# Kernel tuning notes

Measured on AMD Instinct MI355X. Metric: run time of the kernel, lower is better.

## Reference

```python
import jax, jax.numpy as jnp
import numpy as np

B, N, L, D, S, NL = 8, 4096, 32, 64, 64, 2  # batch, stocks, lookback, d_in, d_state, n_levels


def setup_inputs() -> dict:
    key = jax.random.key(0)
    ks = jax.random.split(key, 8)
    w = lambda k, shp: jax.random.normal(k, shp, jnp.float32) * 0.05
    return {
        "p_seq": jax.random.normal(ks[0], (B, N, L, D), jnp.float32),
        "lp_W": w(ks[1], (NL, D, D)),      "lp_b": jnp.zeros((NL, D), jnp.float32),
        "pW":   w(ks[2], (NL, D, 3 * S)),  "pb":   jnp.zeros((NL, 3 * S), jnp.float32),
        "oW":   w(ks[3], (NL, S, S)),      "ob":   jnp.zeros((NL, S), jnp.float32),
        "rW":   w(ks[4], (NL, S, S)),      "rb":   jnp.zeros((NL, S), jnp.float32),
        "fW":   w(ks[5], (NL * S, 1)),     "fb":   jnp.zeros((1,), jnp.float32),
    }


def _gelu(x):
    return jax.nn.gelu(x, approximate=False)  # torch nn.GELU default is exact (erf)


def reference(p_seq, lp_W, lp_b, pW, pb, oW, ob, rW, rb, fW, fb):
    n_levels = lp_W.shape[0]
    feats = []
    for i in range(n_levels):  # small fixed loop over structurally distinct levels
        # level projection: [b,n,l,d]
        x = jnp.einsum('bnld,de->bnle', p_seq, lp_W[i]) + lp_b[i]
        # input-dependent SSM params (per-timestep Linear == one batched matmul)
        p = jnp.einsum('bnld,de->bnle', x, pW[i]) + pb[i]
        a, b_, c = jnp.split(p, 3, axis=-1)
        a = jax.nn.sigmoid(a)
        xm = x.mean(-1, keepdims=True)  # [b,n,l,1]

        # selective recurrence h_t = a_t * h_{t-1} + b_t * mean(x_t), scanned over time
        a_t = jnp.moveaxis(a, 2, 0)    # [l,b,n,s]
        b_t = jnp.moveaxis(b_, 2, 0)
        xm_t = jnp.moveaxis(xm, 2, 0)

        def step(h, inp):
            at, bt, xmt = inp
            return at * h + bt * xmt, None

        h0 = jnp.zeros(a_t.shape[1:], x.dtype)  # [b,n,s]
        h_last, _ = jax.lax.scan(step, h0, (a_t, b_t, xm_t))

        # only the last timestep's output feeds the head (matches original)
        o_last = _gelu(c[:, :, -1, :] * h_last) @ oW[i] + ob[i]
        last = o_last + x[:, :, -1, :].mean(-1, keepdims=True)
        feats.append(last @ rW[i] + rb[i])

    h = jnp.concatenate(feats, axis=-1)  # [b,n, n_levels*s]
    y = (h @ fW + fb).squeeze(-1)        # [b,n]
    return y
```

## Files before the change

### kernel.cpp

```cpp
#include <hip/hip_runtime.h>
#include <hip/hip_bf16.h>
#include <math.h>

using s16x8  = __attribute__((ext_vector_type(8)))  short;
using f32x16 = __attribute__((ext_vector_type(16))) float;

#define BB 8
#define NN 4096
#define LL 32
#define DD 64
#define SS 64
#define NLV 2

#define GRID_BLKS 768
#define NGROUPS   4096

#define WEXT_OFF 0
#define BIAS_OFF 28672
#define WVEC_OFF 29120
#define SIG_OFF  29248
#define BETA_OFF 29250
#define C0_OFF   29252
#define FRAG_OFF 29256
#define FRAG_LDS_BYTES 49152
#define XM_BYTE_OFF    49152

__global__ void prep1(const float* __restrict__ lpW, const float* __restrict__ lpb,
                      const float* __restrict__ pW,  const float* __restrict__ pb,
                      const float* __restrict__ oW,  const float* __restrict__ ob,
                      const float* __restrict__ rW,  const float* __restrict__ rb,
                      const float* __restrict__ fW,  float* __restrict__ ws) {
    __shared__ float q[64];
    int blk = blockIdx.x;
    int d = threadIdx.x;
    if (blk < 2 * 224) {
        int l = blk / 224, j = blk % 224;
        const float* lpWl = lpW + l * 64 * 64;
        const float* pWl  = pW  + l * 64 * 192;
        float wv;
        if (j < 128) {
            int col = j;
            float acc = 0.f;
            for (int e = 0; e < 64; ++e) acc = fmaf(lpWl[d * 64 + e], pWl[e * 192 + col], acc);
            wv = acc;
            if (d == 0) {
                float bb = pb[l * 192 + col];
                for (int e = 0; e < 64; ++e) bb = fmaf(lpb[l * 64 + e], pWl[e * 192 + col], bb);
                ws[BIAS_OFF + l * 224 + j] = bb;
            }
        } else if (j < 160) {
            float s = 0.f;
            for (int e = 0; e < 64; ++e) s += lpWl[d * 64 + e];
            wv = s * (1.f / 64.f);
            if (d == 0) {
                float ss = 0.f;
                for (int e = 0; e < 64; ++e) ss += lpb[l * 64 + e];
                ws[BIAS_OFF + l * 224 + j] = ss * (1.f / 64.f);
            }
        } else {
            int col = j - 32;
            float acc = 0.f;
            for (int e = 0; e < 64; ++e) acc = fmaf(lpWl[d * 64 + e], pWl[e * 192 + col], acc);
            wv = acc;
            if (d == 0) {
                float bb = pb[l * 192 + col];
                for (int e = 0; e < 64; ++e) bb = fmaf(lpb[l * 64 + e], pWl[e * 192 + col], bb);
                ws[BIAS_OFF + l * 224 + j] = bb;
            }
        }
        ws[WEXT_OFF + (l * 64 + d) * 224 + j] = wv;
    } else {
        int l = blk - 2 * 224;
        float qv = 0.f;
        for (int j2 = 0; j2 < 64; ++j2) qv = fmaf(rW[l * 4096 + d * 64 + j2], fW[l * 64 + j2], qv);
        q[d] = qv;
        __syncthreads();
        float wv = 0.f;
        for (int s = 0; s < 64; ++s) wv = fmaf(oW[l * 4096 + d * 64 + s], q[s], wv);
        ws[WVEC_OFF + l * 64 + d] = wv;
        if (d == 0) { float s = 0.f; for (int i = 0; i < 64; ++i) s += q[i];               ws[SIG_OFF  + l] = s; }
        if (d == 1) { float s = 0.f; for (int i = 0; i < 64; ++i) s += ob[l*64+i] * q[i];  ws[BETA_OFF + l] = s; }
        if (d == 2) { float s = 0.f; for (int i = 0; i < 64; ++i) s += rb[l*64+i] * fW[l*64+i]; ws[C0_OFF + l] = s; }
    }
}

__global__ void prep2(float* __restrict__ ws) {
    int blk = blockIdx.x;
    int l = blk / 28, r = blk % 28, nt = r / 4, ks = r % 4;
    int lane = threadIdx.x;
    const float* W = ws + WEXT_OFF + l * 64 * 224;
    s16x8 vh;
#pragma unroll
    for (int i = 0; i < 8; ++i) {
        int k   = ks * 16 + ((lane >> 5) << 2) + (i & 3) + ((i >> 2) << 3);
        int col = nt * 32 + (lane & 31);
        unsigned u = __float_as_uint(W[k * 224 + col]);
        unsigned rn = u + 0x7fffu + ((u >> 16) & 1u);
        vh[i] = (short)(rn >> 16);
    }
    size_t dst;
    if (nt == 4) {
        dst = (size_t)XM_BYTE_OFF + ((size_t)l * 4 + ks) * 1024;
    } else {
        int ntp = (nt < 4) ? nt : nt - 1;
        dst = (((size_t)l * 6 + ntp) * 4 + ks) * 1024;
    }
    char* base = reinterpret_cast<char*>(ws) + (size_t)FRAG_OFF * 4 + dst + lane * 16;
    *reinterpret_cast<s16x8*>(base) = vh;
}

#define BFRD(l, ntp, ks) (*reinterpret_cast<const s16x8*>(smem + ((((l)*6+(ntp))*4+(ks)))*1024 + lane16))

#define ACCINIT(acc, bval) do { float _b = (bval); _Pragma("unroll") \
    for (int _r = 0; _r < 16; ++_r) acc[_r] = _b; } while (0)

#define MMP(l, ntA, ntB, accA, accB) do { _Pragma("unroll") \
    for (int ks = 0; ks < 4; ++ks) { \
        s16x8 bA = BFRD(l, ntA, ks), bB = BFRD(l, ntB, ks); \
        accA = __builtin_amdgcn_mfma_f32_32x32x16_bf16(Ah[ks], bA, accA, 0, 0, 0); \
        accB = __builtin_amdgcn_mfma_f32_32x32x16_bf16(Ah[ks], bB, accB, 0, 0, 0); \
    } } while (0)

#define MX1G(l, acc) do { _Pragma("unroll") \
    for (int ks = 0; ks < 4; ++ks) { \
        s16x8 b = FXM[((l)*4+ks)*64 + lane]; \
        acc = __builtin_amdgcn_mfma_f32_32x32x16_bf16(Ah[ks], b, acc, 0, 0, 0); \
    } } while (0)

__global__ __launch_bounds__(512, 4) void mlm_mfma(
    const float* __restrict__ p_seq, const float* __restrict__ fb,
    const float* __restrict__ ws, float* __restrict__ out) {

    __shared__ __align__(16) char smem[FRAG_LDS_BYTES];
    const int tid  = threadIdx.x;
    const int lane = tid & 63;
    const int wv   = tid >> 6;
    const int lane16 = lane * 16;
    const int row  = lane & 31;
    const int kofs = (lane >> 5) * 4;
    const int myhalf = lane >> 5;
    const int col  = lane & 31;

    const s16x8* __restrict__ FXM = reinterpret_cast<const s16x8*>(
        reinterpret_cast<const char*>(ws) + (size_t)FRAG_OFF * 4 + XM_BYTE_OFF);

    {
        const float4* src = reinterpret_cast<const float4*>(
            reinterpret_cast<const char*>(ws) + (size_t)FRAG_OFF * 4);
        float4* dst = reinterpret_cast<float4*>(smem);
#pragma unroll
        for (int it = 0; it < 6; ++it) dst[tid + it * 512] = src[tid + it * 512];
    }
    __syncthreads();

    auto scan_h = [&](const f32x16& aT, const f32x16& bT, const f32x16& xmT) -> float {
        float Ak[4], Uk[4];
#pragma unroll
        for (int k = 0; k < 4; ++k) {
            const int rb = k * 4;
            float s0 = __builtin_amdgcn_rcpf(1.f + __expf(-aT[rb + 0]));
            float s1 = __builtin_amdgcn_rcpf(1.f + __expf(-aT[rb + 1]));
            float s2 = __builtin_amdgcn_rcpf(1.f + __expf(-aT[rb + 2]));
            float s3 = __builtin_amdgcn_rcpf(1.f + __expf(-aT[rb + 3]));
            float u0 = bT[rb + 0] * xmT[rb + 0];
            float u1 = bT[rb + 1] * xmT[rb + 1];
            float u2 = bT[rb + 2] * xmT[rb + 2];
            float u3 = bT[rb + 3] * xmT[rb + 3];
            float A = (s0 * s1) * (s2 * s3);
            float U = fmaf(fmaf(fmaf(u0, s1, u1), s2, u2), s3, u3);
            float Ao = __shfl_xor(A, 32);
            float Uo = __shfl_xor(U, 32);
            float Ue = myhalf ? Uo : U;
            float Ul = myhalf ? U  : Uo;
            float Al = myhalf ? A  : Ao;
            Ak[k] = A * Ao;
            Uk[k] = fmaf(Ue, Al, Ul);
        }
        float U01 = fmaf(Uk[0], Ak[1], Uk[1]);
        float U23 = fmaf(Uk[2], Ak[3], Uk[3]);
        float A23 = Ak[2] * Ak[3];
        return fmaf(U01, A23, U23);
    };

    const float c0sum = ws[C0_OFF] + ws[C0_OFF + 1] + fb[0];

    for (int g = blockIdx.x; g < NGROUPS; g += GRID_BLKS) {
        const int pair = g * 8 + wv;

        s16x8 Ah[4];
        {
            const float* X = p_seq + (size_t)pair * (LL * DD) + row * 64 + kofs;
#pragma unroll
            for (int ks = 0; ks < 4; ++ks) {
                const float4 v0 = *reinterpret_cast<const float4*>(X + ks * 16);
                const float4 v1 = *reinterpret_cast<const float4*>(X + ks * 16 + 8);
                float f[8] = {v0.x, v0.y, v0.z, v0.w, v1.x, v1.y, v1.z, v1.w};
#pragma unroll
                for (int i = 0; i < 8; ++i) {
                    __hip_bfloat16 b = __float2bfloat16(f[i]);
                    short s; __builtin_memcpy(&s, &b, 2);
                    Ah[ks][i] = s;
                }
            }
        }

        float yp = 0.f;
#pragma unroll 1
        for (int l = 0; l < 2; ++l) {
            const float* bias = ws + BIAS_OFF + l * 224;

            f32x16 xmT; ACCINIT(xmT, bias[128 + col]);
            MX1G(l, xmT);

            f32x16 tA, tB;
            ACCINIT(tA, bias[0 + col]);   ACCINIT(tB, bias[64 + col]);
            MMP(l, 0, 2, tA, tB);
            float h0 = scan_h(tA, tB, xmT);

            ACCINIT(tA, bias[32 + col]);  ACCINIT(tB, bias[96 + col]);
            MMP(l, 1, 3, tA, tB);
            float h1 = scan_h(tA, tB, xmT);

            const float xm31 = xmT[15];
            ACCINIT(tA, bias[160 + col]); ACCINIT(tB, bias[192 + col]);
            MMP(l, 4, 5, tA, tB);

            if (lane >= 32) {
                float x0 = tA[15] * h0;
                float x1 = tB[15] * h1;
                float g0 = 0.5f * x0 * (1.f + erff(x0 * 0.70710678118654752440f));
                float g1 = 0.5f * x1 * (1.f + erff(x1 * 0.70710678118654752440f));
                float term = g0 * ws[WVEC_OFF + l * 64 + (lane - 32)]
                           + g1 * ws[WVEC_OFF + l * 64 + lane];
                if (lane == 32) term += xm31 * ws[SIG_OFF + l] + ws[BETA_OFF + l];
                yp += term;
            }
        }

#pragma unroll
        for (int off = 16; off >= 1; off >>= 1) yp += __shfl_xor(yp, off);
        if (lane == 32) out[pair] = yp + c0sum;
    }
}

extern "C" void kernel_launch(void* const* d_in, const int* in_sizes, int n_in,
                              void* d_out, int out_size, void* d_ws, size_t ws_size,
                              hipStream_t stream) {
    const float* p_seq = (const float*)d_in[0];
    const float* lp_W  = (const float*)d_in[1];
    const float* lp_b  = (const float*)d_in[2];
    const float* pW    = (const float*)d_in[3];
    const float* pb    = (const float*)d_in[4];
    const float* oW    = (const float*)d_in[5];
    const float* ob    = (const float*)d_in[6];
    const float* rW    = (const float*)d_in[7];
    const float* rb    = (const float*)d_in[8];
    const float* fW    = (const float*)d_in[9];
    const float* fb    = (const float*)d_in[10];

    float* ws  = (float*)d_ws;
    float* out = (float*)d_out;

    prep1<<<2 * 224 + 2, 64, 0, stream>>>(lp_W, lp_b, pW, pb, oW, ob, rW, rb, fW, ws);
    prep2<<<2 * 28, 64, 0, stream>>>(ws);

    mlm_mfma<<<GRID_BLKS, 512, 0, stream>>>(p_seq, fb, ws, out);
}
```

Before: 110.0 us.

## Launch one block per group, shrink LDS fragments, and issue input loads before the barrier

Drops the grid-stride persistent loop and launches one 512-thread block per group of 8 (b,n) pairs. Only the a/b weight fragments (32KB) now go into LDS. The xm and c fragments are read from global memory (L2) instead, which should allow more resident blocks per CU. Each wave's p_seq load and bf16 conversion is moved ahead of __syncthreads so it overlaps the LDS staging. In exchange, every one of the 4096 blocks repeats the 32KB LDS fill and pays block launch overhead, and more weight reads hit global memory.

```diff
diff --git a/kernel.cpp b/kernel.cpp
--- a/kernel.cpp
+++ b/kernel.cpp
@@ -11,9 +11,6 @@
 #define DD 64
 #define SS 64
 #define NLV 2
-
-#define GRID_BLKS 768
-#define NGROUPS   4096
 
 #define WEXT_OFF 0
 #define BIAS_OFF 28672
@@ -22,8 +19,8 @@
 #define BETA_OFF 29250
 #define C0_OFF   29252
 #define FRAG_OFF 29256
-#define FRAG_LDS_BYTES 49152
-#define XM_BYTE_OFF    49152
+#define FRAG_LDS_BYTES 32768
+#define G_BYTE_OFF     32768
 
 __global__ void prep1(const float* __restrict__ lpW, const float* __restrict__ lpb,
                       const float* __restrict__ pW,  const float* __restrict__ pb,
@@ -99,17 +96,16 @@
         vh[i] = (short)(rn >> 16);
     }
     size_t dst;
-    if (nt == 4) {
-        dst = (size_t)XM_BYTE_OFF + ((size_t)l * 4 + ks) * 1024;
+    if (nt < 4) {
+        dst = (((size_t)l * 4 + nt) * 4 + ks) * 1024;
     } else {
-        int ntp = (nt < 4) ? nt : nt - 1;
-        dst = (((size_t)l * 6 + ntp) * 4 + ks) * 1024;
+        dst = (size_t)G_BYTE_OFF + (((size_t)l * 3 + (nt - 4)) * 4 + ks) * 1024;
     }
     char* base = reinterpret_cast<char*>(ws) + (size_t)FRAG_OFF * 4 + dst + lane * 16;
     *reinterpret_cast<s16x8*>(base) = vh;
 }
 
-#define BFRD(l, ntp, ks) (*reinterpret_cast<const s16x8*>(smem + ((((l)*6+(ntp))*4+(ks)))*1024 + lane16))
+#define BFRD(l, ntp, ks) (*reinterpret_cast<const s16x8*>(smem + ((((l)*4+(ntp))*4+(ks)))*1024 + lane16))
 
 #define ACCINIT(acc, bval) do { float _b = (bval); _Pragma("unroll") \
     for (int _r = 0; _r < 16; ++_r) acc[_r] = _b; } while (0)
@@ -121,10 +117,18 @@
         accB = __builtin_amdgcn_mfma_f32_32x32x16_bf16(Ah[ks], bB, accB, 0, 0, 0); \
     } } while (0)
 
-#define MX1G(l, acc) do { _Pragma("unroll") \
+#define MXG(l, g, acc) do { _Pragma("unroll") \
     for (int ks = 0; ks < 4; ++ks) { \
-        s16x8 b = FXM[((l)*4+ks)*64 + lane]; \
+        s16x8 b = FG[(((l)*3+(g))*4+ks)*64 + lane]; \
         acc = __builtin_amdgcn_mfma_f32_32x32x16_bf16(Ah[ks], b, acc, 0, 0, 0); \
+    } } while (0)
+
+#define MMG2(l, gA, gB, accA, accB) do { _Pragma("unroll") \
+    for (int ks = 0; ks < 4; ++ks) { \
+        s16x8 bA = FG[(((l)*3+(gA))*4+ks)*64 + lane]; \
+        s16x8 bB = FG[(((l)*3+(gB))*4+ks)*64 + lane]; \
+        accA = __builtin_amdgcn_mfma_f32_32x32x16_bf16(Ah[ks], bA, accA, 0, 0, 0); \
+        accB = __builtin_amdgcn_mfma_f32_32x32x16_bf16(Ah[ks], bB, accB, 0, 0, 0); \
     } } while (0)
 
 __global__ __launch_bounds__(512, 4) void mlm_mfma(
@@ -135,21 +139,39 @@
     const int tid  = threadIdx.x;
     const int lane = tid & 63;
     const int wv   = tid >> 6;
+    const int pair = blockIdx.x * 8 + wv;
     const int lane16 = lane * 16;
     const int row  = lane & 31;
     const int kofs = (lane >> 5) * 4;
     const int myhalf = lane >> 5;
     const int col  = lane & 31;
 
-    const s16x8* __restrict__ FXM = reinterpret_cast<const s16x8*>(
-        reinterpret_cast<const char*>(ws) + (size_t)FRAG_OFF * 4 + XM_BYTE_OFF);
+    const s16x8* __restrict__ FG = reinterpret_cast<const s16x8*>(
+        reinterpret_cast<const char*>(ws) + (size_t)FRAG_OFF * 4 + G_BYTE_OFF);
 
     {
         const float4* src = reinterpret_cast<const float4*>(
             reinterpret_cast<const char*>(ws) + (size_t)FRAG_OFF * 4);
         float4* dst = reinterpret_cast<float4*>(smem);
 #pragma unroll
-        for (int it = 0; it < 6; ++it) dst[tid + it * 512] = src[tid + it * 512];
+        for (int it = 0; it < 4; ++it) dst[tid + it * 512] = src[tid + it * 512];
+    }
+
+    s16x8 Ah[4];
+    {
+        const float* X = p_seq + (size_t)pair * (LL * DD) + row * 64 + kofs;
+#pragma unroll
+        for (int ks = 0; ks < 4; ++ks) {
+            const float4 v0 = *reinterpret_cast<const float4*>(X + ks * 16);
+            const float4 v1 = *reinterpret_cast<const float4*>(X + ks * 16 + 8);
+            float f[8] = {v0.x, v0.y, v0.z, v0.w, v1.x, v1.y, v1.z, v1.w};
+#pragma unroll
+            for (int i = 0; i < 8; ++i) {
+                __hip_bfloat16 b = __float2bfloat16(f[i]);
+                short s; __builtin_memcpy(&s, &b, 2);
+                Ah[ks][i] = s;
+            }
+        }
     }
     __syncthreads();
 
@@ -182,65 +204,44 @@
         return fmaf(U01, A23, U23);
     };
 
+    float yp = 0.f;
     const float c0sum = ws[C0_OFF] + ws[C0_OFF + 1] + fb[0];
 
-    for (int g = blockIdx.x; g < NGROUPS; g += GRID_BLKS) {
-        const int pair = g * 8 + wv;
-
-        s16x8 Ah[4];
-        {
-            const float* X = p_seq + (size_t)pair * (LL * DD) + row * 64 + kofs;
-#pragma unroll
-            for (int ks = 0; ks < 4; ++ks) {
-                const float4 v0 = *reinterpret_cast<const float4*>(X + ks * 16);
-                const float4 v1 = *reinterpret_cast<const float4*>(X + ks * 16 + 8);
-                float f[8] = {v0.x, v0.y, v0.z, v0.w, v1.x, v1.y, v1.z, v1.w};
-#pragma unroll
-                for (int i = 0; i < 8; ++i) {
-                    __hip_bfloat16 b = __float2bfloat16(f[i]);
-                    short s; __builtin_memcpy(&s, &b, 2);
-                    Ah[ks][i] = s;
-                }
-            }
-        }
-
-        float yp = 0.f;
 #pragma unroll 1
-        for (int l = 0; l < 2; ++l) {
-            const float* bias = ws + BIAS_OFF + l * 224;
-
-            f32x16 xmT; ACCINIT(xmT, bias[128 + col]);
-            MX1G(l, xmT);
-
-            f32x16 tA, tB;
-            ACCINIT(tA, bias[0 + col]);   ACCINIT(tB, bias[64 + col]);
-            MMP(l, 0, 2, tA, tB);
-            float h0 = scan_h(tA, tB, xmT);
-
-            ACCINIT(tA, bias[32 + col]);  ACCINIT(tB, bias[96 + col]);
-            MMP(l, 1, 3, tA, tB);
-            float h1 = scan_h(tA, tB, xmT);
-
-            const float xm31 = xmT[15];
-            ACCINIT(tA, bias[160 + col]); ACCINIT(tB, bias[192 + col]);
-            MMP(l, 4, 5, tA, tB);
-
-            if (lane >= 32) {
-                float x0 = tA[15] * h0;
-                float x1 = tB[15] * h1;
-                float g0 = 0.5f * x0 * (1.f + erff(x0 * 0.70710678118654752440f));
-                float g1 = 0.5f * x1 * (1.f + erff(x1 * 0.70710678118654752440f));
-                float term = g0 * ws[WVEC_OFF + l * 64 + (lane - 32)]
-                           + g1 * ws[WVEC_OFF + l * 64 + lane];
-                if (lane == 32) term += xm31 * ws[SIG_OFF + l] + ws[BETA_OFF + l];
-                yp += term;
-            }
-        }
-
-#pragma unroll
-        for (int off = 16; off >= 1; off >>= 1) yp += __shfl_xor(yp, off);
-        if (lane == 32) out[pair] = yp + c0sum;
-    }
+    for (int l = 0; l < 2; ++l) {
+        const float* bias = ws + BIAS_OFF + l * 224;
+
+        f32x16 xmT; ACCINIT(xmT, bias[128 + col]);
+        MXG(l, 0, xmT);
+
+        f32x16 tA, tB;
+        ACCINIT(tA, bias[0 + col]);   ACCINIT(tB, bias[64 + col]);
+        MMP(l, 0, 2, tA, tB);
+        float h0 = scan_h(tA, tB, xmT);
+
+        ACCINIT(tA, bias[32 + col]);  ACCINIT(tB, bias[96 + col]);
+        MMP(l, 1, 3, tA, tB);
+        float h1 = scan_h(tA, tB, xmT);
+
+        const float xm31 = xmT[15];
+        ACCINIT(tA, bias[160 + col]); ACCINIT(tB, bias[192 + col]);
+        MMG2(l, 1, 2, tA, tB);
+
+        if (lane >= 32) {
+            float x0 = tA[15] * h0;
+            float x1 = tB[15] * h1;
+            float g0 = 0.5f * x0 * (1.f + erff(x0 * 0.70710678118654752440f));
+            float g1 = 0.5f * x1 * (1.f + erff(x1 * 0.70710678118654752440f));
+            float term = g0 * ws[WVEC_OFF + l * 64 + (lane - 32)]
+                       + g1 * ws[WVEC_OFF + l * 64 + lane];
+            if (lane == 32) term += xm31 * ws[SIG_OFF + l] + ws[BETA_OFF + l];
+            yp += term;
+        }
+    }
+
+#pragma unroll
+    for (int off = 16; off >= 1; off >>= 1) yp += __shfl_xor(yp, off);
+    if (lane == 32) out[pair] = yp + c0sum;
 }
 
 extern "C" void kernel_launch(void* const* d_in, const int* in_sizes, int n_in,
@@ -264,5 +265,6 @@
     prep1<<<2 * 224 + 2, 64, 0, stream>>>(lp_W, lp_b, pW, pb, oW, ob, rW, rb, fW, ws);
     prep2<<<2 * 28, 64, 0, stream>>>(ws);
 
-    mlm_mfma<<<GRID_BLKS, 512, 0, stream>>>(p_seq, fb, ws, out);
-}
+    const int pairs = BB * NN;
+    mlm_mfma<<<pairs / 8, 512, 0, stream>>>(p_seq, fb, ws, out);
+}
```

New measurement: 110.0 us. About the same (-0.0%).
